# Kernel tuning notes

Hardware: AMD Instinct MI355X
Metric: run time of the kernel (lower is better)

Reference implementation:

```python
import jax, jax.numpy as jnp
import numpy as np
from jax import lax

T, IN, H, OUT = 8192, 1, 1024, 1


def setup_inputs() -> dict:
    key = jax.random.key(0)
    ks = jax.random.split(key, 7)
    s = 1.0 / np.sqrt(H)
    return {
        "x": jax.random.normal(ks[0], (T, IN), dtype=jnp.float32),
        "W_ih": jax.random.uniform(ks[1], (4 * H, IN), jnp.float32, -s, s),
        "W_hh": jax.random.uniform(ks[2], (4 * H, H), jnp.float32, -s, s),
        "b_ih": jax.random.uniform(ks[3], (4 * H,), jnp.float32, -s, s),
        "b_hh": jax.random.uniform(ks[4], (4 * H,), jnp.float32, -s, s),
        "W_fc": jax.random.uniform(ks[5], (OUT, H), jnp.float32, -s, s),
        "b_fc": jax.random.uniform(ks[6], (OUT,), jnp.float32, -s, s),
    }


def reference(x, W_ih, W_hh, b_ih, b_hh, W_fc, b_fc):
    # x: (T, input_size); batch dim of 1 is squeezed out.
    H_ = W_hh.shape[1]
    # Precompute input contribution to all gates for every timestep: (T, 4H)
    xg = x @ W_ih.T + (b_ih + b_hh)

    def step(carry, gx):
        h, c = carry
        g = gx + h @ W_hh.T  # (4H,) -- PyTorch gate order i, f, g, o
        i, f, gg, o = jnp.split(g, 4)
        c = jax.nn.sigmoid(f) * c + jax.nn.sigmoid(i) * jnp.tanh(gg)
        h = jax.nn.sigmoid(o) * jnp.tanh(c)
        return (h, c), h

    h0 = jnp.zeros((H_,), dtype=x.dtype)
    c0 = jnp.zeros((H_,), dtype=x.dtype)
    _, hs = lax.scan(step, (h0, c0), xg)  # hs: (T, H)
    return hs @ W_fc.T + b_fc  # (T, output_size)
```

## Files before the change

### kernel.cpp

```cpp
#include <hip/hip_runtime.h>

#define TT    8192
#define HD    1024
#define NBLK  256
#define NTHR  256
#define NBUF  4
#define NREP  8

typedef int i32x4 __attribute__((ext_vector_type(4)));
typedef int i32x2 __attribute__((ext_vector_type(2)));

__device__ __forceinline__ void llc_load_pair(const unsigned* p, i32x4& a, i32x4& b) {
  asm volatile("global_load_dwordx4 %0, %2, off sc0 sc1\n\t"
               "global_load_dwordx4 %1, %3, off sc0 sc1\n\t"
               "s_waitcnt vmcnt(0)"
               : "=&v"(a), "=&v"(b)
               : "v"(p), "v"(p + 4)
               : "memory");
}
__device__ __forceinline__ unsigned llc_load1(const unsigned* p) {
  unsigned r;
  asm volatile("global_load_dword %0, %1, off sc0 sc1\n\ts_waitcnt vmcnt(0)"
               : "=v"(r) : "v"(p) : "memory");
  return r;
}
__device__ __forceinline__ void llc_store2(unsigned* p, unsigned lo, unsigned hi) {
  i32x2 v; v.x = (int)lo; v.y = (int)hi;
  asm volatile("global_store_dwordx2 %0, %1, off sc0 sc1"
               :: "v"(p), "v"(v) : "memory");
}
__device__ __forceinline__ void llc_store1(unsigned* p, unsigned v) {
  asm volatile("global_store_dword %0, %1, off sc0 sc1"
               :: "v"(p), "v"(v) : "memory");
}

__device__ __forceinline__ float sigf(float z) {
  return 1.0f / (1.0f + __expf(-z));
}
__device__ __forceinline__ float tanh_fast(float z) {
  float az = fabsf(z);
  float e  = __expf(2.0f * az);
  float t  = 1.0f - 2.0f / (e + 1.0f);
  return z < 0.0f ? -t : t;
}

#define FMA4(acc, hvv, wvv)                                      \
  acc = fmaf((hvv).x, (wvv).x, acc);                             \
  acc = fmaf((hvv).y, (wvv).y, acc);                             \
  acc = fmaf((hvv).z, (wvv).z, acc);                             \
  acc = fmaf((hvv).w, (wvv).w, acc);

extern "C" __global__ __launch_bounds__(NTHR, 1)
void lstm_persistent(const float* __restrict__ x,
                     const float* __restrict__ W_ih,
                     const float* __restrict__ W_hh,
                     const float* __restrict__ b_ih,
                     const float* __restrict__ b_hh,
                     const float* __restrict__ W_fc,
                     const float* __restrict__ b_fc,
                     float* __restrict__ out,
                     unsigned* __restrict__ flag,
                     unsigned* __restrict__ hbuf)
{
  const int tid = threadIdx.x;
  const int blk = blockIdx.x;

  if (blk == NBLK) {
    for (int t = 0; t < TT; ++t) {
      const unsigned* src = hbuf + (((t & (NBUF - 1)) * HD + tid * 4) * 2);
      i32x4 A, B;
      const int want = t + 1;
      do {
        llc_load_pair(src, A, B);
      } while (!(A.y == want && A.w == want && B.y == want && B.w == want));
      __syncthreads();
      if (tid < NREP)
        llc_store1(flag + (tid << 4), (unsigned)want);
    }
    return;
  }

  __shared__ float x_lds[TT];
  __shared__ float h_lds[HD];

  const int wave = tid >> 6;
  const int lane = tid & 63;
  const int g    = lane >> 4;
  const int kc   = lane & 15;
  const int unit = blk * 4 + wave;

  for (int i = tid; i < TT / 4; i += NTHR)
    ((float4*)x_lds)[i] = ((const float4*)x)[i];

  float4 w4[16];
  {
    const float* wr = W_hh + (size_t)(g * HD + unit) * HD + kc * 4;
#pragma unroll
    for (int m = 0; m < 16; ++m)
      w4[m] = *((const float4*)(wr + m * 64));
  }
  float4 wfc4[4];
#pragma unroll
  for (int m = 0; m < 4; ++m)
    wfc4[m] = *((const float4*)(W_fc + m * 256 + lane * 4));
  const float bfc_val = b_fc[0];

  float wih_g[4], bs_g[4];
#pragma unroll
  for (int q = 0; q < 4; ++q) {
    int r = q * HD + unit;
    wih_g[q] = W_ih[r];
    bs_g[q]  = b_ih[r] + b_hh[r];
  }
  float c_state = 0.0f;
  __syncthreads();

  const unsigned* flag_mine = flag + ((blk & (NREP - 1)) << 4);

  for (int t = 0; t < TT; ++t) {
    const bool doproj = (t > 0) && (wave == 1) && (blk == (t & 255));
    float accs = 0.0f;
    float4 hp4[4];

    if (t > 0) {
      while (llc_load1(flag_mine) < (unsigned)t) { }
      const unsigned* src = hbuf + (((t - 1) & (NBUF - 1)) * HD + tid * 4) * 2;
      i32x4 A, B;
      llc_load_pair(src, A, B);
      float4 hv;
      hv.x = __int_as_float(A.x); hv.y = __int_as_float(A.z);
      hv.z = __int_as_float(B.x); hv.w = __int_as_float(B.z);
      ((float4*)h_lds)[tid] = hv;
      __syncthreads();

      const float* hp = h_lds + kc * 4;
      float s0 = 0.f, s1 = 0.f, s2 = 0.f, s3 = 0.f;
#pragma unroll
      for (int mb = 0; mb < 4; ++mb) {
        float4 ha = *((const float4*)(hp + (mb * 4 + 0) * 64));
        float4 hb = *((const float4*)(hp + (mb * 4 + 1) * 64));
        float4 hc = *((const float4*)(hp + (mb * 4 + 2) * 64));
        float4 hd = *((const float4*)(hp + (mb * 4 + 3) * 64));
        FMA4(s0, ha, w4[mb * 4 + 0]);
        FMA4(s1, hb, w4[mb * 4 + 1]);
        FMA4(s2, hc, w4[mb * 4 + 2]);
        FMA4(s3, hd, w4[mb * 4 + 3]);
      }
      accs = (s0 + s1) + (s2 + s3);

      if (doproj) {
#pragma unroll
        for (int m = 0; m < 4; ++m)
          hp4[m] = *((const float4*)(h_lds + m * 256 + lane * 4));
      }
    }

#pragma unroll
    for (int s = 1; s < 16; s <<= 1)
      accs += __shfl_xor(accs, s);

    float gi = __shfl(accs, 0);
    float gf = __shfl(accs, 16);
    float gg = __shfl(accs, 32);
    float go = __shfl(accs, 48);

    if (lane == 0) {
      float xt = x_lds[t];
      gi += fmaf(xt, wih_g[0], bs_g[0]);
      gf += fmaf(xt, wih_g[1], bs_g[1]);
      gg += fmaf(xt, wih_g[2], bs_g[2]);
      go += fmaf(xt, wih_g[3], bs_g[3]);
      c_state  = sigf(gf) * c_state + sigf(gi) * tanh_fast(gg);
      float hn = sigf(go) * tanh_fast(c_state);
      llc_store2(hbuf + (((t & (NBUF - 1)) * HD + unit) * 2),
                 __float_as_uint(hn), (unsigned)(t + 1));
    }

    if (doproj) {
      float p = 0.f;
#pragma unroll
      for (int m = 0; m < 4; ++m) { FMA4(p, hp4[m], wfc4[m]); }
#pragma unroll
      for (int s = 1; s < 64; s <<= 1) p += __shfl_xor(p, s);
      if (lane == 0) out[t - 1] = p + bfc_val;
    }
  }

  if (blk == 0) {
    const unsigned* src = hbuf + (((TT - 1) & (NBUF - 1)) * HD + tid * 4) * 2;
    i32x4 A, B;
    do {
      llc_load_pair(src, A, B);
    } while (!(A.y == TT && A.w == TT && B.y == TT && B.w == TT));
    float4 hv;
    hv.x = __int_as_float(A.x); hv.y = __int_as_float(A.z);
    hv.z = __int_as_float(B.x); hv.w = __int_as_float(B.z);
    ((float4*)h_lds)[tid] = hv;
    __syncthreads();
    if (wave == 1) {
      float p = 0.f;
#pragma unroll
      for (int m = 0; m < 4; ++m) {
        float4 hm = *((const float4*)(h_lds + m * 256 + lane * 4));
        FMA4(p, hm, wfc4[m]);
      }
#pragma unroll
      for (int s = 1; s < 64; s <<= 1) p += __shfl_xor(p, s);
      if (lane == 0) out[TT - 1] = p + bfc_val;
    }
  }
}

extern "C" void kernel_launch(void* const* d_in, const int* in_sizes, int n_in,
                              void* d_out, int out_size, void* d_ws, size_t ws_size,
                              hipStream_t stream) {
  const float* x   = (const float*)d_in[0];
  const float* Wih = (const float*)d_in[1];
  const float* Whh = (const float*)d_in[2];
  const float* bih = (const float*)d_in[3];
  const float* bhh = (const float*)d_in[4];
  const float* Wfc = (const float*)d_in[5];
  const float* bfc = (const float*)d_in[6];
  float* out = (float*)d_out;

  unsigned* flag = (unsigned*)d_ws;
  unsigned* hbuf = flag + NREP * 16;
  size_t init_bytes = (NREP * 16 + NBUF * HD * 2) * sizeof(unsigned);

  hipMemsetAsync(d_ws, 0, init_bytes, stream);
  hipLaunchKernelGGL(lstm_persistent, dim3(NBLK + 1), dim3(NTHR), 0, stream,
                     x, Wih, Whh, bih, bhh, Wfc, bfc, out, flag, hbuf);
}
```

Before: 23.17 ms.

## Replace aggregator-block flag barrier with direct per-element tagged polling of h

Removes the extra aggregator block that polled the hidden-state buffer and broadcast a replicated step flag. Each block now spins directly on the step-tagged h values it needs, which cuts one global round-trip per timestep from the serial critical path. The output projection moves to a fifth wave that has its own LDS buffer, and h_lds is double-buffered so the projection runs off the recurrence path. The cost is 256 blocks each polling all of hbuf every step, which adds heavy L2/LLC contention, plus a larger block size.

```diff
diff --git a/kernel.cpp b/kernel.cpp
--- a/kernel.cpp
+++ b/kernel.cpp
@@ -3,9 +3,8 @@
 #define TT    8192
 #define HD    1024
 #define NBLK  256
-#define NTHR  256
+#define NTHR  320
 #define NBUF  4
-#define NREP  8
 
 typedef int i32x4 __attribute__((ext_vector_type(4)));
 typedef int i32x2 __attribute__((ext_vector_type(2)));
@@ -18,19 +17,9 @@
                : "v"(p), "v"(p + 4)
                : "memory");
 }
-__device__ __forceinline__ unsigned llc_load1(const unsigned* p) {
-  unsigned r;
-  asm volatile("global_load_dword %0, %1, off sc0 sc1\n\ts_waitcnt vmcnt(0)"
-               : "=v"(r) : "v"(p) : "memory");
-  return r;
-}
 __device__ __forceinline__ void llc_store2(unsigned* p, unsigned lo, unsigned hi) {
   i32x2 v; v.x = (int)lo; v.y = (int)hi;
   asm volatile("global_store_dwordx2 %0, %1, off sc0 sc1"
-               :: "v"(p), "v"(v) : "memory");
-}
-__device__ __forceinline__ void llc_store1(unsigned* p, unsigned v) {
-  asm volatile("global_store_dword %0, %1, off sc0 sc1"
                :: "v"(p), "v"(v) : "memory");
 }
 
@@ -59,29 +48,13 @@
                      const float* __restrict__ W_fc,
                      const float* __restrict__ b_fc,
                      float* __restrict__ out,
-                     unsigned* __restrict__ flag,
                      unsigned* __restrict__ hbuf)
 {
   const int tid = threadIdx.x;
   const int blk = blockIdx.x;
 
-  if (blk == NBLK) {
-    for (int t = 0; t < TT; ++t) {
-      const unsigned* src = hbuf + (((t & (NBUF - 1)) * HD + tid * 4) * 2);
-      i32x4 A, B;
-      const int want = t + 1;
-      do {
-        llc_load_pair(src, A, B);
-      } while (!(A.y == want && A.w == want && B.y == want && B.w == want));
-      __syncthreads();
-      if (tid < NREP)
-        llc_store1(flag + (tid << 4), (unsigned)want);
-    }
-    return;
-  }
-
   __shared__ float x_lds[TT];
-  __shared__ float h_lds[HD];
+  __shared__ float h_lds[2][HD];
 
   const int wave = tid >> 6;
   const int lane = tid & 63;
@@ -93,115 +66,120 @@
     ((float4*)x_lds)[i] = ((const float4*)x)[i];
 
   float4 w4[16];
-  {
+  float  wih_g[4], bs_g[4];
+  float4 wfc4[4];
+  float  bfc_val = 0.0f;
+
+  if (wave < 4) {
     const float* wr = W_hh + (size_t)(g * HD + unit) * HD + kc * 4;
 #pragma unroll
     for (int m = 0; m < 16; ++m)
       w4[m] = *((const float4*)(wr + m * 64));
-  }
-  float4 wfc4[4];
-#pragma unroll
-  for (int m = 0; m < 4; ++m)
-    wfc4[m] = *((const float4*)(W_fc + m * 256 + lane * 4));
-  const float bfc_val = b_fc[0];
-
-  float wih_g[4], bs_g[4];
-#pragma unroll
-  for (int q = 0; q < 4; ++q) {
-    int r = q * HD + unit;
-    wih_g[q] = W_ih[r];
-    bs_g[q]  = b_ih[r] + b_hh[r];
+#pragma unroll
+    for (int q = 0; q < 4; ++q) {
+      int r = q * HD + unit;
+      wih_g[q] = W_ih[r];
+      bs_g[q]  = b_ih[r] + b_hh[r];
+    }
+  } else {
+#pragma unroll
+    for (int m = 0; m < 4; ++m)
+      wfc4[m] = *((const float4*)(W_fc + m * 256 + lane * 4));
+    bfc_val = b_fc[0];
   }
   float c_state = 0.0f;
   __syncthreads();
 
-  const unsigned* flag_mine = flag + ((blk & (NREP - 1)) << 4);
-
   for (int t = 0; t < TT; ++t) {
-    const bool doproj = (t > 0) && (wave == 1) && (blk == (t & 255));
     float accs = 0.0f;
-    float4 hp4[4];
 
     if (t > 0) {
-      while (llc_load1(flag_mine) < (unsigned)t) { }
-      const unsigned* src = hbuf + (((t - 1) & (NBUF - 1)) * HD + tid * 4) * 2;
+      if (tid < 256) {
+        const unsigned* src =
+            hbuf + (((t - 1) & (NBUF - 1)) * HD + tid * 4) * 2;
+        const int want = t;
+        i32x4 A, B;
+        do {
+          llc_load_pair(src, A, B);
+        } while (!(A.y == want && A.w == want && B.y == want && B.w == want));
+        float4 hv;
+        hv.x = __int_as_float(A.x); hv.y = __int_as_float(A.z);
+        hv.z = __int_as_float(B.x); hv.w = __int_as_float(B.z);
+        ((float4*)h_lds[t & 1])[tid] = hv;
+      }
+      __syncthreads();
+
+      if (wave < 4) {
+        const float* hp = h_lds[t & 1] + kc * 4;
+        float s0 = 0.f, s1 = 0.f, s2 = 0.f, s3 = 0.f;
+#pragma unroll
+        for (int mb = 0; mb < 4; ++mb) {
+          float4 ha = *((const float4*)(hp + (mb * 4 + 0) * 64));
+          float4 hb = *((const float4*)(hp + (mb * 4 + 1) * 64));
+          float4 hc = *((const float4*)(hp + (mb * 4 + 2) * 64));
+          float4 hd = *((const float4*)(hp + (mb * 4 + 3) * 64));
+          FMA4(s0, ha, w4[mb * 4 + 0]);
+          FMA4(s1, hb, w4[mb * 4 + 1]);
+          FMA4(s2, hc, w4[mb * 4 + 2]);
+          FMA4(s3, hd, w4[mb * 4 + 3]);
+        }
+        accs = (s0 + s1) + (s2 + s3);
+      } else if (blk == ((t - 1) & 255)) {
+        float p = 0.f;
+#pragma unroll
+        for (int m = 0; m < 4; ++m) {
+          float4 hm = *((const float4*)(h_lds[t & 1] + m * 256 + lane * 4));
+          FMA4(p, hm, wfc4[m]);
+        }
+#pragma unroll
+        for (int s = 1; s < 64; s <<= 1) p += __shfl_xor(p, s);
+        if (lane == 0) out[t - 1] = p + bfc_val;
+      }
+    }
+
+    if (wave < 4) {
+#pragma unroll
+      for (int s = 1; s < 16; s <<= 1)
+        accs += __shfl_xor(accs, s);
+
+      float gi = __shfl(accs, 0);
+      float gf = __shfl(accs, 16);
+      float gg = __shfl(accs, 32);
+      float go = __shfl(accs, 48);
+
+      if (lane == 0) {
+        float xt = x_lds[t];
+        gi += fmaf(xt, wih_g[0], bs_g[0]);
+        gf += fmaf(xt, wih_g[1], bs_g[1]);
+        gg += fmaf(xt, wih_g[2], bs_g[2]);
+        go += fmaf(xt, wih_g[3], bs_g[3]);
+        c_state  = sigf(gf) * c_state + sigf(gi) * tanh_fast(gg);
+        float hn = sigf(go) * tanh_fast(c_state);
+        llc_store2(hbuf + (((t & (NBUF - 1)) * HD + unit) * 2),
+                   __float_as_uint(hn), (unsigned)(t + 1));
+      }
+    }
+  }
+
+  if (blk == ((TT - 1) & 255)) {
+    if (tid < 256) {
+      const unsigned* src =
+          hbuf + (((TT - 1) & (NBUF - 1)) * HD + tid * 4) * 2;
       i32x4 A, B;
-      llc_load_pair(src, A, B);
+      do {
+        llc_load_pair(src, A, B);
+      } while (!(A.y == TT && A.w == TT && B.y == TT && B.w == TT));
       float4 hv;
       hv.x = __int_as_float(A.x); hv.y = __int_as_float(A.z);
       hv.z = __int_as_float(B.x); hv.w = __int_as_float(B.z);
-      ((float4*)h_lds)[tid] = hv;
-      __syncthreads();
-
-      const float* hp = h_lds + kc * 4;
-      float s0 = 0.f, s1 = 0.f, s2 = 0.f, s3 = 0.f;
-#pragma unroll
-      for (int mb = 0; mb < 4; ++mb) {
-        float4 ha = *((const float4*)(hp + (mb * 4 + 0) * 64));
-        float4 hb = *((const float4*)(hp + (mb * 4 + 1) * 64));
-        float4 hc = *((const float4*)(hp + (mb * 4 + 2) * 64));
-        float4 hd = *((const float4*)(hp + (mb * 4 + 3) * 64));
-        FMA4(s0, ha, w4[mb * 4 + 0]);
-        FMA4(s1, hb, w4[mb * 4 + 1]);
-        FMA4(s2, hc, w4[mb * 4 + 2]);
-        FMA4(s3, hd, w4[mb * 4 + 3]);
-      }
-      accs = (s0 + s1) + (s2 + s3);
-
-      if (doproj) {
-#pragma unroll
-        for (int m = 0; m < 4; ++m)
-          hp4[m] = *((const float4*)(h_lds + m * 256 + lane * 4));
-      }
-    }
-
-#pragma unroll
-    for (int s = 1; s < 16; s <<= 1)
-      accs += __shfl_xor(accs, s);
-
-    float gi = __shfl(accs, 0);
-    float gf = __shfl(accs, 16);
-    float gg = __shfl(accs, 32);
-    float go = __shfl(accs, 48);
-
-    if (lane == 0) {
-      float xt = x_lds[t];
-      gi += fmaf(xt, wih_g[0], bs_g[0]);
-      gf += fmaf(xt, wih_g[1], bs_g[1]);
-      gg += fmaf(xt, wih_g[2], bs_g[2]);
-      go += fmaf(xt, wih_g[3], bs_g[3]);
-      c_state  = sigf(gf) * c_state + sigf(gi) * tanh_fast(gg);
-      float hn = sigf(go) * tanh_fast(c_state);
-      llc_store2(hbuf + (((t & (NBUF - 1)) * HD + unit) * 2),
-                 __float_as_uint(hn), (unsigned)(t + 1));
-    }
-
-    if (doproj) {
+      ((float4*)h_lds[0])[tid] = hv;
+    }
+    __syncthreads();
+    if (wave == 4) {
       float p = 0.f;
 #pragma unroll
-      for (int m = 0; m < 4; ++m) { FMA4(p, hp4[m], wfc4[m]); }
-#pragma unroll
-      for (int s = 1; s < 64; s <<= 1) p += __shfl_xor(p, s);
-      if (lane == 0) out[t - 1] = p + bfc_val;
-    }
-  }
-
-  if (blk == 0) {
-    const unsigned* src = hbuf + (((TT - 1) & (NBUF - 1)) * HD + tid * 4) * 2;
-    i32x4 A, B;
-    do {
-      llc_load_pair(src, A, B);
-    } while (!(A.y == TT && A.w == TT && B.y == TT && B.w == TT));
-    float4 hv;
-    hv.x = __int_as_float(A.x); hv.y = __int_as_float(A.z);
-    hv.z = __int_as_float(B.x); hv.w = __int_as_float(B.z);
-    ((float4*)h_lds)[tid] = hv;
-    __syncthreads();
-    if (wave == 1) {
-      float p = 0.f;
-#pragma unroll
       for (int m = 0; m < 4; ++m) {
-        float4 hm = *((const float4*)(h_lds + m * 256 + lane * 4));
+        float4 hm = *((const float4*)(h_lds[0] + m * 256 + lane * 4));
         FMA4(p, hm, wfc4[m]);
       }
 #pragma unroll
@@ -223,11 +201,10 @@
   const float* bfc = (const float*)d_in[6];
   float* out = (float*)d_out;
 
-  unsigned* flag = (unsigned*)d_ws;
-  unsigned* hbuf = flag + NREP * 16;
-  size_t init_bytes = (NREP * 16 + NBUF * HD * 2) * sizeof(unsigned);
+  unsigned* hbuf = (unsigned*)d_ws;
+  size_t init_bytes = (size_t)(NBUF * HD * 2) * sizeof(unsigned);
 
   hipMemsetAsync(d_ws, 0, init_bytes, stream);
-  hipLaunchKernelGGL(lstm_persistent, dim3(NBLK + 1), dim3(NTHR), 0, stream,
-                     x, Wih, Whh, bih, bhh, Wfc, bfc, out, flag, hbuf);
-}
+  hipLaunchKernelGGL(lstm_persistent, dim3(NBLK), dim3(NTHR), 0, stream,
+                     x, Wih, Whh, bih, bhh, Wfc, bfc, out, hbuf);
+}
```

Result: slower. 34.41 ms (+48.5%).
